# Performance work log

Hardware: AMD Instinct MI355X
Metric: run time of the kernel (lower is better)

Reference implementation:

```python
import jax, jax.numpy as jnp
import numpy as np

# GDN (gated delta-rule) linear attention, prefill path, single packed sequence,
# no initial conv/ssm state.
NUM_K_HEADS = 16
NUM_V_HEADS = 32
HEAD_K_DIM = 128
HEAD_V_DIM = 128
HIDDEN = 2048
CONV_K = 4
EPS = 1e-6
K_TOTAL = NUM_K_HEADS * HEAD_K_DIM
V_TOTAL = NUM_V_HEADS * HEAD_V_DIM
QKV_TOTAL = 2 * K_TOTAL + V_TOTAL


def setup_inputs() -> dict:
    key = jax.random.key(0)
    ks = jax.random.split(key, 9)
    T = 2048
    s = 0.02
    return {
        "hidden_states": jax.random.normal(ks[0], (T, HIDDEN), jnp.float32),
        "in_proj_qkv_weight": s * jax.random.normal(ks[1], (QKV_TOTAL, HIDDEN), jnp.float32),
        "in_proj_z_weight": s * jax.random.normal(ks[2], (V_TOTAL, HIDDEN), jnp.float32),
        "in_proj_a_weight": s * jax.random.normal(ks[3], (NUM_V_HEADS, HIDDEN), jnp.float32),
        "in_proj_b_weight": s * jax.random.normal(ks[4], (NUM_V_HEADS, HIDDEN), jnp.float32),
        "conv1d_weight": 0.1 * jax.random.normal(ks[5], (QKV_TOTAL, CONV_K), jnp.float32),
        "out_proj_weight": s * jax.random.normal(ks[6], (HIDDEN, V_TOTAL), jnp.float32),
        "norm_weight": jnp.ones((HEAD_V_DIM,), jnp.float32),
        "A_log": jnp.log(jnp.linspace(1.0, 8.0, NUM_V_HEADS, dtype=jnp.float32)),
        "dt_bias": 0.5 * jax.random.normal(ks[7], (NUM_V_HEADS,), jnp.float32),
    }


def _causal_conv1d_silu(x, w):
    # x: [T, C], w: [C, K] depthwise causal conv + SiLU
    T = x.shape[0]
    K = w.shape[1]
    xp = jnp.pad(x, ((K - 1, 0), (0, 0)))
    y = xp[0:T] * w[:, 0]
    for j in range(1, K):  # small fixed K
        y = y + xp[j:j + T] * w[:, j]
    return jax.nn.silu(y)


def _l2norm(x):
    return x / jnp.sqrt(jnp.sum(x * x, axis=-1, keepdims=True) + EPS)


def _gdn_recurrence(q, k, v, g, beta, scale):
    # q,k: [T,Hv,Dk] (l2-normed, repeated over GQA groups), v: [T,Hv,Dv]
    # g,beta: [T,Hv]. State S: [Hv,Dk,Dv]. Gated delta rule:
    #   S <- exp(g)*S ; S <- S + k^T beta (v - k S) ; o = scale * q S
    Hv, Dk = q.shape[1], q.shape[2]
    Dv = v.shape[2]

    def step(S, inp):
        q_t, k_t, v_t, g_t, b_t = inp
        S = S * jnp.exp(g_t)[:, None, None]
        pred = jnp.einsum('hk,hkv->hv', k_t, S)
        delta = b_t[:, None] * (v_t - pred)
        S = S + jnp.einsum('hk,hv->hkv', k_t, delta)
        o = jnp.einsum('hk,hkv->hv', q_t * scale, S)
        return S, o

    S0 = jnp.zeros((Hv, Dk, Dv), q.dtype)
    _, o = jax.lax.scan(step, S0, (q, k, v, g, beta))
    return o  # [T,Hv,Dv]


def reference(hidden_states, in_proj_qkv_weight, in_proj_z_weight, in_proj_a_weight,
              in_proj_b_weight, conv1d_weight, out_proj_weight, norm_weight, A_log, dt_bias):
    T = hidden_states.shape[0]
    mixed = hidden_states @ in_proj_qkv_weight.T            # [T, QKV_TOTAL]
    z = hidden_states @ in_proj_z_weight.T                  # [T, V_TOTAL]
    a = hidden_states @ in_proj_a_weight.T                  # [T, Hv]
    b = hidden_states @ in_proj_b_weight.T                  # [T, Hv]

    mixed = _causal_conv1d_silu(mixed, conv1d_weight)

    q, k, v = jnp.split(mixed, [K_TOTAL, 2 * K_TOTAL], axis=-1)
    q = q.reshape(T, NUM_K_HEADS, HEAD_K_DIM)
    k = k.reshape(T, NUM_K_HEADS, HEAD_K_DIM)
    v = v.reshape(T, NUM_V_HEADS, HEAD_V_DIM)

    # qk l2-norm in kernel, GQA repeat to v heads
    q = _l2norm(q)
    k = _l2norm(k)
    ratio = NUM_V_HEADS // NUM_K_HEADS
    q = jnp.repeat(q, ratio, axis=1)
    k = jnp.repeat(k, ratio, axis=1)

    # fused_gdn_gating: g = -exp(A_log) * softplus(a + dt_bias); beta = sigmoid(b)
    g = -jnp.exp(A_log) * jax.nn.softplus(a + dt_bias)      # [T,Hv]
    beta = jax.nn.sigmoid(b)                                # [T,Hv]

    o = _gdn_recurrence(q, k, v, g, beta, HEAD_K_DIM ** -0.5)  # [T,Hv,Dv]

    # gated RMSNorm: rmsnorm(o) * norm_weight * silu(z)
    o = o * jax.lax.rsqrt(jnp.mean(o * o, axis=-1, keepdims=True) + EPS) * norm_weight
    o = o * jax.nn.silu(z.reshape(T, NUM_V_HEADS, HEAD_V_DIM))

    return o.reshape(T, -1) @ out_proj_weight.T             # [T, HIDDEN]
```

## Files before the change

### kernel.cpp

```cpp
#include <hip/hip_runtime.h>
#include <math.h>

#define T_SEQ     2048
#define HIDDEN_D  2048
#define NUM_KH    16
#define NUM_VH    32
#define HEAD_DIM  128
#define K_TOTAL   2048
#define V_TOTAL   4096
#define QKV_TOTAL 8192
#define EPS_F     1e-6f
#define CC        32
#define NCHUNK    (T_SEQ / CC)
#define NV        8

typedef __attribute__((ext_vector_type(4))) float f32x4;
typedef __attribute__((ext_vector_type(8))) short s16x8;
typedef __attribute__((ext_vector_type(8))) unsigned short u16x8;

__device__ __forceinline__ unsigned short f2bf(float f) {
    unsigned int u = __float_as_uint(f);
    u += 0x7FFFu + ((u >> 16) & 1u);
    return (unsigned short)(u >> 16);
}

__device__ __forceinline__ float bf2f(unsigned short h) {
    return __uint_as_float((unsigned int)h << 16);
}

__global__ __launch_bounds__(256) void cast_bf16_kernel(
    const float* __restrict__ src, unsigned short* __restrict__ dst, int n4)
{
    int idx = blockIdx.x * 256 + threadIdx.x;
    if (idx >= n4) return;
    float4 v = ((const float4*)src)[idx];
    ushort4 o;
    o.x = f2bf(v.x); o.y = f2bf(v.y); o.z = f2bf(v.z); o.w = f2bf(v.w);
    ((ushort4*)dst)[idx] = o;
}

__global__ __launch_bounds__(256) void gemm_bt_bf16(
    const unsigned short* __restrict__ A, const unsigned short* __restrict__ B,
    float* __restrict__ C, int M, int N, int K)
{
    __shared__ unsigned short As[128 * 64];
    __shared__ unsigned short Bs[128 * 64];
    const int tid  = threadIdx.x;
    const int wave = tid >> 6;
    const int lane = tid & 63;
    const int m0 = blockIdx.y * 128;
    const int n0 = blockIdx.x * 128;
    const int wm = (wave >> 1) * 64;
    const int wn = (wave & 1) * 64;

    f32x4 acc[4][4];
    f32x4 zero = {0.f, 0.f, 0.f, 0.f};
#pragma unroll
    for (int i = 0; i < 4; ++i)
#pragma unroll
        for (int j = 0; j < 4; ++j) acc[i][j] = zero;

    const int srow = lane >> 3;
    const int scol = (lane & 7) * 8;
    const int rm = lane & 15;
    const int koq = (lane >> 4) * 8;

    for (int kt = 0; kt < K; kt += 64) {
#pragma unroll
        for (int l = 0; l < 4; ++l) {
            const int r0 = wave * 32 + l * 8;
            const unsigned short* ga =
                A + (size_t)(m0 + r0 + srow) * K + kt + scol;
            const unsigned short* gb =
                B + (size_t)(n0 + r0 + srow) * K + kt + scol;
            __builtin_amdgcn_global_load_lds(
                (const __attribute__((address_space(1))) void*)ga,
                (__attribute__((address_space(3))) void*)&As[r0 * 64], 16, 0, 0);
            __builtin_amdgcn_global_load_lds(
                (const __attribute__((address_space(1))) void*)gb,
                (__attribute__((address_space(3))) void*)&Bs[r0 * 64], 16, 0, 0);
        }
        __syncthreads();

#pragma unroll
        for (int ks = 0; ks < 2; ++ks) {
            const int ko = ks * 32 + koq;
            s16x8 af[4], bfr[4];
#pragma unroll
            for (int i = 0; i < 4; ++i) {
                af[i]  = *(const s16x8*)&As[(wm + i * 16 + rm) * 64 + ko];
                bfr[i] = *(const s16x8*)&Bs[(wn + i * 16 + rm) * 64 + ko];
            }
#pragma unroll
            for (int i = 0; i < 4; ++i)
#pragma unroll
                for (int j = 0; j < 4; ++j)
                    acc[i][j] = __builtin_amdgcn_mfma_f32_16x16x32_bf16(
                        af[i], bfr[j], acc[i][j], 0, 0, 0);
        }
        __syncthreads();
    }

    const int cr = (lane >> 4) * 4;
    const int ccol = lane & 15;
#pragma unroll
    for (int i = 0; i < 4; ++i)
#pragma unroll
        for (int j = 0; j < 4; ++j) {
#pragma unroll
            for (int r = 0; r < 4; ++r)
                C[(size_t)(m0 + wm + i * 16 + cr + r) * N
                  + n0 + wn + j * 16 + ccol] = acc[i][j][r];
        }
}

__global__ __launch_bounds__(256) void gemm_nt_64(
    const float* __restrict__ A, const float* __restrict__ B,
    float* __restrict__ C, int M, int N, int K)
{
    __shared__ float As[16][68];
    __shared__ float Bs[16][68];
    const int tid = threadIdx.x;
    const int m0 = blockIdx.y * 64;
    const int n0 = blockIdx.x * 64;
    const int tm = tid >> 4;
    const int tn = tid & 15;
    const int lr = tid >> 2;
    const int lc = (tid & 3) * 4;

    float acc[4][4];
#pragma unroll
    for (int i = 0; i < 4; ++i)
#pragma unroll
        for (int j = 0; j < 4; ++j) acc[i][j] = 0.f;

    for (int kt = 0; kt < K; kt += 16) {
        float4 av = *(const float4*)(A + (size_t)(m0 + lr) * K + kt + lc);
        float4 bv = *(const float4*)(B + (size_t)(n0 + lr) * K + kt + lc);
        As[lc + 0][lr] = av.x; As[lc + 1][lr] = av.y;
        As[lc + 2][lr] = av.z; As[lc + 3][lr] = av.w;
        Bs[lc + 0][lr] = bv.x; Bs[lc + 1][lr] = bv.y;
        Bs[lc + 2][lr] = bv.z; Bs[lc + 3][lr] = bv.w;
        __syncthreads();
#pragma unroll
        for (int kk = 0; kk < 16; ++kk) {
            float4 a4 = *(const float4*)&As[kk][tm * 4];
            float4 b4 = *(const float4*)&Bs[kk][tn * 4];
            float a[4] = {a4.x, a4.y, a4.z, a4.w};
            float b[4] = {b4.x, b4.y, b4.z, b4.w};
#pragma unroll
            for (int i = 0; i < 4; ++i)
#pragma unroll
                for (int j = 0; j < 4; ++j)
                    acc[i][j] = fmaf(a[i], b[j], acc[i][j]);
        }
        __syncthreads();
    }
#pragma unroll
    for (int i = 0; i < 4; ++i) {
        float4 o = make_float4(acc[i][0], acc[i][1], acc[i][2], acc[i][3]);
        *(float4*)(C + (size_t)(m0 + tm * 4 + i) * N + n0 + tn * 4) = o;
    }
}

__global__ __launch_bounds__(256) void concat_ab_kernel(
    const float* __restrict__ Wa, const float* __restrict__ Wb,
    float* __restrict__ Wab)
{
    int idx = blockIdx.x * 256 + threadIdx.x;
    int half = 16384;
    const float* src = (idx < half) ? Wa : Wb;
    int off = (idx < half) ? idx : idx - half;
    ((float4*)Wab)[idx] = ((const float4*)src)[off];
}

__global__ __launch_bounds__(256) void gating_finalize_kernel(
    const float* __restrict__ ab, const float* __restrict__ A_log,
    const float* __restrict__ dt_bias, float* __restrict__ g,
    float* __restrict__ beta)
{
    int idx = blockIdx.x * 256 + threadIdx.x;
    int t = idx >> 5, h = idx & 31;
    float a = ab[t * 64 + h] + dt_bias[h];
    float b = ab[t * 64 + 32 + h];
    float sp = (a > 20.f) ? a : log1pf(expf(a));
    g[idx] = -expf(A_log[h]) * sp;
    beta[idx] = 1.f / (1.f + expf(-b));
}

__global__ __launch_bounds__(256) void conv_v_kernel(
    const float* __restrict__ mixed, const float* __restrict__ cw,
    float* __restrict__ vb)
{
    int idx = blockIdx.x * 256 + threadIdx.x;
    int c = idx & (V_TOTAL - 1);
    int t = idx >> 12;
    int ch = 2 * K_TOTAL + c;
    const float4 w = *(const float4*)(cw + (size_t)ch * 4);
    const float* base = mixed + (size_t)t * QKV_TOTAL + ch;
    float y = w.w * base[0];
    if (t >= 1) y = fmaf(w.z, base[-QKV_TOTAL], y);
    if (t >= 2) y = fmaf(w.y, base[-2 * QKV_TOTAL], y);
    if (t >= 3) y = fmaf(w.x, base[-3 * QKV_TOTAL], y);
    vb[idx] = y / (1.f + expf(-y));
}

__global__ __launch_bounds__(64) void convqk_l2_kernel(
    const float* __restrict__ mixed, const float* __restrict__ cw,
    unsigned short* __restrict__ qk_bf)
{
    const int row = blockIdx.x;
    const int t = row >> 5;
    const int r = row & 31;
    const int lane = threadIdx.x;
    const int c = r * HEAD_DIM + lane * 2;
    const float4 w0 = *(const float4*)(cw + (size_t)c * 4);
    const float4 w1 = *(const float4*)(cw + (size_t)(c + 1) * 4);
    const float* base = mixed + (size_t)t * QKV_TOTAL + c;
    float2 x0 = *(const float2*)base;
    float y0 = w0.w * x0.x, y1 = w1.w * x0.y;
    if (t >= 1) {
        float2 x = *(const float2*)(base - QKV_TOTAL);
        y0 = fmaf(w0.z, x.x, y0); y1 = fmaf(w1.z, x.y, y1);
    }
    if (t >= 2) {
        float2 x = *(const float2*)(base - 2 * QKV_TOTAL);
        y0 = fmaf(w0.y, x.x, y0); y1 = fmaf(w1.y, x.y, y1);
    }
    if (t >= 3) {
        float2 x = *(const float2*)(base - 3 * QKV_TOTAL);
        y0 = fmaf(w0.x, x.x, y0); y1 = fmaf(w1.x, x.y, y1);
    }
    y0 = y0 / (1.f + expf(-y0));
    y1 = y1 / (1.f + expf(-y1));
    float s = y0 * y0 + y1 * y1;
    for (int off = 32; off > 0; off >>= 1) s += __shfl_down(s, off);
    s = __shfl(s, 0);
    float inv = rsqrtf(s + EPS_F);
    unsigned short* qb = qk_bf + (size_t)t * 4096 + c;
    qb[0] = f2bf(y0 * inv);
    qb[1] = f2bf(y1 * inv);
}

__global__ __launch_bounds__(256) void gdn_p1(
    const unsigned short* __restrict__ qk_bf, const float* __restrict__ g,
    const float* __restrict__ beta, unsigned short* __restrict__ PTbuf,
    unsigned short* __restrict__ K2buf, float* __restrict__ lam_g,
    float* __restrict__ bet_g)
{
    __shared__ float Kn[CC][132];
    __shared__ float Qn[CC][132];
    __shared__ float Wm[CC][33];
    __shared__ float Tld[CC][36];
    __shared__ float Pm[CC][33];
    __shared__ float Trl[CC][33];
    __shared__ float cums[CC];
    __shared__ float betas[CC];
    __shared__ float rlS[CC];

    const int tid = threadIdx.x;
    const int h   = blockIdx.x;
    const int cix = blockIdx.y;
    const int t0  = cix * CC;
    const int kh  = h >> 1;
    const float scale = 0.08838834764831845f;
    const size_t mb = ((size_t)cix * NUM_VH + h);
    const size_t sb = mb * CC;

    if (tid < CC) {
        float x = g[(size_t)(t0 + tid) * NUM_VH + h];
        float bv = beta[(size_t)(t0 + tid) * NUM_VH + h];
#pragma unroll
        for (int off = 1; off < 32; off <<= 1) {
            float n = __shfl_up(x, off);
            if (tid >= off) x += n;
        }
        cums[tid] = x;
        betas[tid] = bv;
        float c31 = __shfl(x, 31);
        lam_g[sb + tid] = expf(x);
        bet_g[sb + tid] = bv;
        rlS[tid] = expf(c31 - x);
    }
#pragma unroll
    for (int p = 0; p < 2; ++p) {
        int idx = p * 256 + tid;
        int i = idx >> 4, ch = (idx & 15) * 8;
        const unsigned short* qr =
            qk_bf + (size_t)(t0 + i) * 4096 + kh * HEAD_DIM + ch;
        u16x8 q8 = *(const u16x8*)qr;
        u16x8 k8 = *(const u16x8*)(qr + K_TOTAL);
        float4 kf0, kf1, qf0, qf1;
        kf0.x = bf2f(k8[0]); kf0.y = bf2f(k8[1]);
        kf0.z = bf2f(k8[2]); kf0.w = bf2f(k8[3]);
        kf1.x = bf2f(k8[4]); kf1.y = bf2f(k8[5]);
        kf1.z = bf2f(k8[6]); kf1.w = bf2f(k8[7]);
        qf0.x = bf2f(q8[0]) * scale; qf0.y = bf2f(q8[1]) * scale;
        qf0.z = bf2f(q8[2]) * scale; qf0.w = bf2f(q8[3]) * scale;
        qf1.x = bf2f(q8[4]) * scale; qf1.y = bf2f(q8[5]) * scale;
        qf1.z = bf2f(q8[6]) * scale; qf1.w = bf2f(q8[7]) * scale;
        *(float4*)&Kn[i][ch]     = kf0;
        *(float4*)&Kn[i][ch + 4] = kf1;
        *(float4*)&Qn[i][ch]     = qf0;
        *(float4*)&Qn[i][ch + 4] = qf1;
    }
    __syncthreads();

    {
        const int i0 = (tid >> 4) * 2, j0 = (tid & 15) * 2;
        float wa[2][2] = {{0.f, 0.f}, {0.f, 0.f}};
        float pa[2][2] = {{0.f, 0.f}, {0.f, 0.f}};
        for (int k = 0; k < HEAD_DIM; k += 4) {
            float4 a0 = *(const float4*)&Kn[i0][k];
            float4 a1 = *(const float4*)&Kn[i0 + 1][k];
            float4 b0 = *(const float4*)&Kn[j0][k];
            float4 b1 = *(const float4*)&Kn[j0 + 1][k];
            float4 c0 = *(const float4*)&Qn[i0][k];
            float4 c1 = *(const float4*)&Qn[i0 + 1][k];
            const float* ap0 = (const float*)&a0;
            const float* ap1 = (const float*)&a1;
            const float* bp0 = (const float*)&b0;
            const float* bp1 = (const float*)&b1;
            const float* cp0 = (const float*)&c0;
            const float* cp1 = (const float*)&c1;
#pragma unroll
            for (int cc = 0; cc < 4; ++cc) {
                wa[0][0] = fmaf(ap0[cc], bp0[cc], wa[0][0]);
                wa[0][1] = fmaf(ap0[cc], bp1[cc], wa[0][1]);
                wa[1][0] = fmaf(ap1[cc], bp0[cc], wa[1][0]);
                wa[1][1] = fmaf(ap1[cc], bp1[cc], wa[1][1]);
                pa[0][0] = fmaf(cp0[cc], bp0[cc], pa[0][0]);
                pa[0][1] = fmaf(cp0[cc], bp1[cc], pa[0][1]);
                pa[1][0] = fmaf(cp1[cc], bp0[cc], pa[1][0]);
                pa[1][1] = fmaf(cp1[cc], bp1[cc], pa[1][1]);
            }
        }
#pragma unroll
        for (int di = 0; di < 2; ++di)
#pragma unroll
            for (int dj = 0; dj < 2; ++dj) {
                int i = i0 + di, j = j0 + dj;
                float rr = expf(fminf(cums[i] - cums[j], 0.f));
                Wm[i][j] = (j < i) ? betas[i] * rr * wa[di][dj] : 0.f;
                Pm[i][j] = (j <= i) ? rr * pa[di][dj] : 0.f;
            }
    }
    __syncthreads();

    {
        const int col = tid >> 3, tk = tid & 7;
        if (tk == 0) Tld[0][col] = (col == 0) ? 1.f : 0.f;
        for (int i = 1; i < CC; ++i) {
            float part = 0.f;
            for (int j = tk; j < i; j += 8)
                part = fmaf(Wm[i][j], Tld[j][col], part);
            part += __shfl_xor(part, 4);
            part += __shfl_xor(part, 2);
            part += __shfl_xor(part, 1);
            if (tk == 0) Tld[i][col] = ((i == col) ? 1.f : 0.f) - part;
        }
    }
    __syncthreads();

    {
        const int i = tid >> 3, j0 = (tid & 7) * 4;
        const float r = rlS[i];
#pragma unroll
        for (int e = 0; e < 4; ++e)
            Trl[i][j0 + e] = Tld[i][j0 + e] * r;
        float4 accp = {0.f, 0.f, 0.f, 0.f};
        for (int m = 0; m < CC; ++m) {
            float pv = Pm[i][m];
            float4 tv = *(const float4*)&Tld[m][j0];
            accp.x = fmaf(pv, tv.x, accp.x);
            accp.y = fmaf(pv, tv.y, accp.y);
            accp.z = fmaf(pv, tv.z, accp.z);
            accp.w = fmaf(pv, tv.w, accp.w);
        }
        ushort4 pt4;
        pt4.x = f2bf(accp.x); pt4.y = f2bf(accp.y);
        pt4.z = f2bf(accp.z); pt4.w = f2bf(accp.w);
        *(ushort4*)(PTbuf + mb * (CC * CC) + tid * 4) = pt4;
    }
    __syncthreads();

    {
        const int m0 = tid >> 3;
        const int q  = (tid & 7) * 4;
        float acc[4][4];
#pragma unroll
        for (int c = 0; c < 4; ++c)
#pragma unroll
            for (int e = 0; e < 4; ++e) acc[c][e] = 0.f;
        for (int j = 0; j < CC; ++j) {
            float t = Trl[j][m0];
#pragma unroll
            for (int c = 0; c < 4; ++c) {
                float4 a = *(const float4*)&Kn[j][q + 32 * c];
                acc[c][0] = fmaf(t, a.x, acc[c][0]);
                acc[c][1] = fmaf(t, a.y, acc[c][1]);
                acc[c][2] = fmaf(t, a.z, acc[c][2]);
                acc[c][3] = fmaf(t, a.w, acc[c][3]);
            }
        }
        unsigned short* kout =
            K2buf + mb * (CC * HEAD_DIM) + m0 * HEAD_DIM + q;
#pragma unroll
        for (int c = 0; c < 4; ++c) {
            ushort4 o4;
            o4.x = f2bf(acc[c][0]); o4.y = f2bf(acc[c][1]);
            o4.z = f2bf(acc[c][2]); o4.w = f2bf(acc[c][3]);
            *(ushort4*)(kout + 32 * c) = o4;
        }
    }
}

__global__ __launch_bounds__(256, 2) void gdn_p2(
    const float* __restrict__ vb, const unsigned short* __restrict__ qk_bf,
    const unsigned short* __restrict__ PTbuf,
    const unsigned short* __restrict__ K2buf, const float* __restrict__ lam_g,
    const float* __restrict__ bet_g, float* __restrict__ o)
{
    __shared__ unsigned short Kn[CC][128];
    __shared__ unsigned short Qn[CC][128];
    __shared__ unsigned short K2l[2][CC][128];
    __shared__ float PTl[2][CC][36];
    __shared__ float Sm[HEAD_DIM][NV + 2];
    __shared__ float Dl[CC][NV + 2];
    __shared__ float lamS[2][CC], betS[2][CC];

    const int tid = threadIdx.x;
    const int wv  = tid >> 6;
    const int ln  = tid & 63;
    const int h   = blockIdx.x >> 4;
    const int V0  = (blockIdx.x & 15) * NV;
    const int kh  = h >> 1;
    const float scale = 0.08838834764831845f;

    const int ri = tid >> 3;
    const int rn = (tid & 3) * 2;
    const int hh = (tid >> 2) & 1;
    const int rx2 = ri & 3;

    const int fk = (tid >> 3) * 4;
    const int sn = tid & 7;

    const int drow = ln >> 4;
    const int dc   = ln & 15;

#define DMA_KQ(T0)                                                            \
    {                                                                         \
        _Pragma("unroll")                                                     \
        for (int p = 0; p < 2; ++p) {                                         \
            const int i = p * 16 + wv * 4 + drow;                             \
            const int sc = 2 * ((dc >> 1) ^ (i & 3)) + (dc & 1);              \
            const unsigned short* sq = qk_bf + (size_t)((T0) + i) * 4096      \
                                       + kh * HEAD_DIM + sc * 8;              \
            __builtin_amdgcn_global_load_lds(                                 \
                (const __attribute__((address_space(1))) void*)(sq + K_TOTAL),\
                (__attribute__((address_space(3))) void*)                     \
                    &Kn[p * 16 + wv * 4][0], 16, 0, 0);                       \
            __builtin_amdgcn_global_load_lds(                                 \
                (const __attribute__((address_space(1))) void*)sq,            \
                (__attribute__((address_space(3))) void*)                     \
                    &Qn[p * 16 + wv * 4][0], 16, 0, 0);                       \
        }                                                                     \
    }

#define DMA_K2(MB, BUF)                                                       \
    {                                                                         \
        _Pragma("unroll")                                                     \
        for (int p = 0; p < 2; ++p) {                                         \
            const unsigned short* sk = K2buf + (MB) * (CC * HEAD_DIM)         \
                                       + p * 2048 + wv * 512 + ln * 8;        \
            __builtin_amdgcn_global_load_lds(                                 \
                (const __attribute__((address_space(1))) void*)sk,            \
                (__attribute__((address_space(3))) void*)                     \
                    &K2l[BUF][p * 16 + wv * 4][0], 16, 0, 0);                 \
        }                                                                     \
    }

#pragma unroll
    for (int c = 0; c < 4; ++c) Sm[fk + c][sn] = 0.f;

    DMA_KQ(0);
    DMA_K2((size_t)h, 0);
    {
        ushort4 pt0 = *(const ushort4*)(PTbuf + (size_t)h * (CC * CC) + tid * 4);
        float4 pf;
        pf.x = bf2f(pt0.x); pf.y = bf2f(pt0.y);
        pf.z = bf2f(pt0.z); pf.w = bf2f(pt0.w);
        *(float4*)&PTl[0][tid >> 3][(tid & 7) * 4] = pf;
        if (tid < CC) {
            lamS[0][tid] = lam_g[(size_t)h * CC + tid];
            betS[0][tid] = bet_g[(size_t)h * CC + tid];
        }
    }
    float2 vR = *(const float2*)(vb + (size_t)ri * V_TOTAL
                                 + h * HEAD_DIM + V0 + rn);

    int cur = 0;
    for (int cix = 0; cix < NCHUNK; ++cix) {
        const int t0 = cix * CC;
        __syncthreads();

        const float lam = lamS[cur][ri];
        const float bet = betS[cur][ri];
        float r1x = 0.f, r1y = 0.f, r2x = 0.f, r2y = 0.f;
#pragma unroll
        for (int kk = 0; kk < 8; ++kk) {
            const int pc = (2 * (kk ^ rx2) + hh) * 8;
            const int cl = kk * 16 + hh * 8;
            u16x8 kv = *(const u16x8*)&Kn[ri][pc];
            u16x8 qv = *(const u16x8*)&Qn[ri][pc];
#pragma unroll
            for (int c8 = 0; c8 < 8; ++c8) {
                float kf = bf2f(kv[c8]);
                float qf = bf2f(qv[c8]);
                float2 s = *(const float2*)&Sm[cl + c8][rn];
                r1x = fmaf(kf, s.x, r1x);
                r1y = fmaf(kf, s.y, r1y);
                r2x = fmaf(qf, s.x, r2x);
                r2y = fmaf(qf, s.y, r2y);
            }
        }
        r1x += __shfl_xor(r1x, 4);
        r1y += __shfl_xor(r1y, 4);
        r2x += __shfl_xor(r2x, 4);
        r2y += __shfl_xor(r2y, 4);
        {
            float dlx = bet * (vR.x - lam * r1x);
            float dly = bet * (vR.y - lam * r1y);
            if (hh == 0) { Dl[ri][rn] = dlx; Dl[ri][rn + 1] = dly; }
        }
        const float lsc = lam * scale;
        float ox = r2x * lsc, oy = r2y * lsc;
        __syncthreads();

        const int nxt = cur ^ 1;
        ushort4 ptN; float lamN = 0.f, betN = 0.f; float2 vN;
        const int more = (cix + 1 < NCHUNK);
        if (more) {
            const int t0n = t0 + CC;
            const size_t mbn = (size_t)(cix + 1) * NUM_VH + h;
            DMA_KQ(t0n);
            DMA_K2(mbn, nxt);
            ptN = *(const ushort4*)(PTbuf + mbn * (CC * CC) + tid * 4);
            if (tid < CC) {
                lamN = lam_g[mbn * CC + tid];
                betN = bet_g[mbn * CC + tid];
            }
            vN = *(const float2*)(vb + (size_t)(t0n + ri) * V_TOTAL
                                  + h * HEAD_DIM + V0 + rn);
        }

        {
            for (int j = 0; j < CC; ++j) {
                float p = PTl[cur][ri][j];
                float2 d = *(const float2*)&Dl[j][rn];
                ox = fmaf(p, d.x, ox);
                oy = fmaf(p, d.y, oy);
            }
            if (hh == 0)
                *(float2*)(o + (size_t)(t0 + ri) * V_TOTAL + h * HEAD_DIM + V0 + rn)
                    = make_float2(ox, oy);
        }

        {
            const float lamL = lamS[cur][CC - 1];
            float s0 = lamL * Sm[fk + 0][sn];
            float s1 = lamL * Sm[fk + 1][sn];
            float s2 = lamL * Sm[fk + 2][sn];
            float s3 = lamL * Sm[fk + 3][sn];
            for (int j = 0; j < CC; ++j) {
                ushort4 kk = *(const ushort4*)&K2l[cur][j][fk];
                float d = Dl[j][sn];
                s0 = fmaf(bf2f(kk.x), d, s0);
                s1 = fmaf(bf2f(kk.y), d, s1);
                s2 = fmaf(bf2f(kk.z), d, s2);
                s3 = fmaf(bf2f(kk.w), d, s3);
            }
            Sm[fk + 0][sn] = s0;
            Sm[fk + 1][sn] = s1;
            Sm[fk + 2][sn] = s2;
            Sm[fk + 3][sn] = s3;
        }

        if (more) {
            float4 pf;
            pf.x = bf2f(ptN.x); pf.y = bf2f(ptN.y);
            pf.z = bf2f(ptN.z); pf.w = bf2f(ptN.w);
            *(float4*)&PTl[nxt][tid >> 3][(tid & 7) * 4] = pf;
            if (tid < CC) { lamS[nxt][tid] = lamN; betS[nxt][tid] = betN; }
            vR = vN;
        }
        cur = nxt;
    }
#undef DMA_KQ
#undef DMA_K2
}

__global__ __launch_bounds__(64) void rmsnorm_gate_kernel(
    float* __restrict__ o, const float* __restrict__ z,
    const float* __restrict__ nw)
{
    const int row = blockIdx.x;
    float* p = o + (size_t)row * HEAD_DIM;
    const float* zp = z + (size_t)row * HEAD_DIM;
    const int lane = threadIdx.x;
    float2 v = *(float2*)(p + lane * 2);
    float s = v.x * v.x + v.y * v.y;
    for (int off = 32; off > 0; off >>= 1) s += __shfl_down(s, off);
    s = __shfl(s, 0);
    float inv = rsqrtf(s * (1.f / HEAD_DIM) + EPS_F);
    float2 zv = *(float2*)(zp + lane * 2);
    float2 wv = *(const float2*)(nw + lane * 2);
    v.x = v.x * inv * wv.x * (zv.x / (1.f + expf(-zv.x)));
    v.y = v.y * inv * wv.y * (zv.y / (1.f + expf(-zv.y)));
    *(float2*)(p + lane * 2) = v;
}

extern "C" void kernel_launch(void* const* d_in, const int* in_sizes, int n_in,
                              void* d_out, int out_size, void* d_ws,
                              size_t ws_size, hipStream_t stream)
{
    const float* hs    = (const float*)d_in[0];
    const float* Wqkv  = (const float*)d_in[1];
    const float* Wz    = (const float*)d_in[2];
    const float* Wa    = (const float*)d_in[3];
    const float* Wb    = (const float*)d_in[4];
    const float* cw    = (const float*)d_in[5];
    const float* Wout  = (const float*)d_in[6];
    const float* nw    = (const float*)d_in[7];
    const float* A_log = (const float*)d_in[8];
    const float* dtb   = (const float*)d_in[9];
    float* out = (float*)d_out;

    float* F     = (float*)d_ws;
    float* mixed = F;
    float* ob    = F;
    unsigned short* PTbuf = (unsigned short*)(F + (size_t)8388608);
    unsigned short* K2buf = (unsigned short*)(F + (size_t)9437184);
    float* lam_b = F + (size_t)13631488;
    float* bet_b = F + (size_t)13697024;
    unsigned short* hs_bf   = (unsigned short*)(F + (size_t)16777216);
    unsigned short* Wqkv_bf = (unsigned short*)(F + (size_t)18874368);
    float* vb = F + (size_t)16777216;
    unsigned short* qk_bf = (unsigned short*)(F + (size_t)25165824);
    unsigned short* Wz_bf   = (unsigned short*)(F + (size_t)27262976);
    float* Wab = F + (size_t)27262976;
    float* ab  = F + (size_t)27394048;
    float* zb  = F + (size_t)33554432;
    unsigned short* ob_bf   = (unsigned short*)(F + (size_t)33554432);
    unsigned short* Wout_bf = (unsigned short*)(F + (size_t)37748736);
    float* gb = F + (size_t)41943040;
    float* bb = F + (size_t)42008576;

    cast_bf16_kernel<<<1048576 / 256, 256, 0, stream>>>(hs, hs_bf, 1048576);
    cast_bf16_kernel<<<4194304 / 256, 256, 0, stream>>>(Wqkv, Wqkv_bf, 4194304);
    cast_bf16_kernel<<<2097152 / 256, 256, 0, stream>>>(Wz, Wz_bf, 2097152);
    gemm_bt_bf16<<<dim3(QKV_TOTAL / 128, T_SEQ / 128), 256, 0, stream>>>(
        hs_bf, Wqkv_bf, mixed, T_SEQ, QKV_TOTAL, HIDDEN_D);
    gemm_bt_bf16<<<dim3(V_TOTAL / 128, T_SEQ / 128), 256, 0, stream>>>(
        hs_bf, Wz_bf, zb, T_SEQ, V_TOTAL, HIDDEN_D);
    concat_ab_kernel<<<32768 / 256, 256, 0, stream>>>(Wa, Wb, Wab);
    gemm_nt_64<<<dim3(1, T_SEQ / 64), 256, 0, stream>>>(
        hs, Wab, ab, T_SEQ, 64, HIDDEN_D);
    gating_finalize_kernel<<<(T_SEQ * NUM_VH) / 256, 256, 0, stream>>>(
        ab, A_log, dtb, gb, bb);
    conv_v_kernel<<<(T_SEQ * V_TOTAL) / 256, 256, 0, stream>>>(
        mixed, cw, vb);
    convqk_l2_kernel<<<T_SEQ * 32, 64, 0, stream>>>(mixed, cw, qk_bf);
    gdn_p1<<<dim3(NUM_VH, NCHUNK), 256, 0, stream>>>(
        qk_bf, gb, bb, PTbuf, K2buf, lam_b, bet_b);
    gdn_p2<<<NUM_VH * (HEAD_DIM / NV), 256, 0, stream>>>(
        vb, qk_bf, PTbuf, K2buf, lam_b, bet_b, ob);
    rmsnorm_gate_kernel<<<T_SEQ * NUM_VH, 64, 0, stream>>>(ob, zb, nw);
    cast_bf16_kernel<<<2097152 / 256, 256, 0, stream>>>(ob, ob_bf, 2097152);
    cast_bf16_kernel<<<2097152 / 256, 256, 0, stream>>>(Wout, Wout_bf, 2097152);
    gemm_bt_bf16<<<dim3(HIDDEN_D / 128, T_SEQ / 128), 256, 0, stream>>>(
        ob_bf, Wout_bf, out, T_SEQ, HIDDEN_D, V_TOTAL);
}
```

Baseline: 929.4 us.

## Fuse input casts, fold bf16 cast into rmsnorm, remap gdn_p2 threads

Merges the three fp32-to-bf16 input casts into a single launch and has the gated RMSNorm kernel write bf16 directly, which removes a separate cast kernel and one fp32 round trip of the output buffer. In the recurrence kernel, each thread now handles two rows and a quarter of the K dimension, so each Sm load is reused across two rows, at the cost of a two-step shuffle reduction and more registers. The ob_bf buffer moves to the PTbuf region, which is free once gdn_p2 has finished.

```diff
diff --git a/kernel.cpp b/kernel.cpp
--- a/kernel.cpp
+++ b/kernel.cpp
@@ -37,6 +37,22 @@
     ushort4 o;
     o.x = f2bf(v.x); o.y = f2bf(v.y); o.z = f2bf(v.z); o.w = f2bf(v.w);
     ((ushort4*)dst)[idx] = o;
+}
+
+__global__ __launch_bounds__(256) void cast3_kernel(
+    const float* __restrict__ hs, const float* __restrict__ Wqkv,
+    const float* __restrict__ Wz, unsigned short* __restrict__ hs_bf,
+    unsigned short* __restrict__ Wqkv_bf, unsigned short* __restrict__ Wz_bf)
+{
+    int idx = blockIdx.x * 256 + threadIdx.x;
+    const float* src; unsigned short* dst; int off;
+    if (idx < 1048576)      { src = hs;   dst = hs_bf;   off = idx; }
+    else if (idx < 5242880) { src = Wqkv; dst = Wqkv_bf; off = idx - 1048576; }
+    else                    { src = Wz;   dst = Wz_bf;   off = idx - 5242880; }
+    float4 v = ((const float4*)src)[off];
+    ushort4 o;
+    o.x = f2bf(v.x); o.y = f2bf(v.y); o.z = f2bf(v.z); o.w = f2bf(v.w);
+    ((ushort4*)dst)[off] = o;
 }
 
 __global__ __launch_bounds__(256) void gemm_bt_bf16(
@@ -437,10 +453,10 @@
     const int kh  = h >> 1;
     const float scale = 0.08838834764831845f;
 
-    const int ri = tid >> 3;
-    const int rn = (tid & 3) * 2;
-    const int hh = (tid >> 2) & 1;
-    const int rx2 = ri & 3;
+    const int hh  = tid & 3;
+    const int rn2 = ((tid >> 2) & 3) * 2;
+    const int rp  = tid >> 4;
+    const int rx  = rp & 3;
 
     const int fk = (tid >> 3) * 4;
     const int sn = tid & 7;
@@ -496,49 +512,66 @@
             betS[0][tid] = bet_g[(size_t)h * CC + tid];
         }
     }
-    float2 vR = *(const float2*)(vb + (size_t)ri * V_TOTAL
-                                 + h * HEAD_DIM + V0 + rn);
+    float2 vR0 = *(const float2*)(vb + (size_t)rp * V_TOTAL
+                                  + h * HEAD_DIM + V0 + rn2);
+    float2 vR1 = *(const float2*)(vb + (size_t)(rp + 16) * V_TOTAL
+                                  + h * HEAD_DIM + V0 + rn2);
 
     int cur = 0;
     for (int cix = 0; cix < NCHUNK; ++cix) {
         const int t0 = cix * CC;
         __syncthreads();
 
-        const float lam = lamS[cur][ri];
-        const float bet = betS[cur][ri];
-        float r1x = 0.f, r1y = 0.f, r2x = 0.f, r2y = 0.f;
-#pragma unroll
-        for (int kk = 0; kk < 8; ++kk) {
-            const int pc = (2 * (kk ^ rx2) + hh) * 8;
-            const int cl = kk * 16 + hh * 8;
-            u16x8 kv = *(const u16x8*)&Kn[ri][pc];
-            u16x8 qv = *(const u16x8*)&Qn[ri][pc];
+        const float lam0 = lamS[cur][rp];
+        const float lam1 = lamS[cur][rp + 16];
+        const float bet0 = betS[cur][rp];
+        const float bet1 = betS[cur][rp + 16];
+        float r1x0 = 0.f, r1y0 = 0.f, r2x0 = 0.f, r2y0 = 0.f;
+        float r1x1 = 0.f, r1y1 = 0.f, r2x1 = 0.f, r2y1 = 0.f;
+#pragma unroll
+        for (int j = 0; j < 4; ++j) {
+            const int c  = 4 * j + hh;
+            const int pc = (2 * ((c >> 1) ^ rx) + (c & 1)) * 8;
+            u16x8 kv0 = *(const u16x8*)&Kn[rp][pc];
+            u16x8 qv0 = *(const u16x8*)&Qn[rp][pc];
+            u16x8 kv1 = *(const u16x8*)&Kn[rp + 16][pc];
+            u16x8 qv1 = *(const u16x8*)&Qn[rp + 16][pc];
+            const int kb = c * 8;
 #pragma unroll
             for (int c8 = 0; c8 < 8; ++c8) {
-                float kf = bf2f(kv[c8]);
-                float qf = bf2f(qv[c8]);
-                float2 s = *(const float2*)&Sm[cl + c8][rn];
-                r1x = fmaf(kf, s.x, r1x);
-                r1y = fmaf(kf, s.y, r1y);
-                r2x = fmaf(qf, s.x, r2x);
-                r2y = fmaf(qf, s.y, r2y);
-            }
-        }
-        r1x += __shfl_xor(r1x, 4);
-        r1y += __shfl_xor(r1y, 4);
-        r2x += __shfl_xor(r2x, 4);
-        r2y += __shfl_xor(r2y, 4);
+                float2 s = *(const float2*)&Sm[kb + c8][rn2];
+                float k0 = bf2f(kv0[c8]), q0 = bf2f(qv0[c8]);
+                float k1 = bf2f(kv1[c8]), q1 = bf2f(qv1[c8]);
+                r1x0 = fmaf(k0, s.x, r1x0); r1y0 = fmaf(k0, s.y, r1y0);
+                r2x0 = fmaf(q0, s.x, r2x0); r2y0 = fmaf(q0, s.y, r2y0);
+                r1x1 = fmaf(k1, s.x, r1x1); r1y1 = fmaf(k1, s.y, r1y1);
+                r2x1 = fmaf(q1, s.x, r2x1); r2y1 = fmaf(q1, s.y, r2y1);
+            }
+        }
+        r1x0 += __shfl_xor(r1x0, 1); r1x0 += __shfl_xor(r1x0, 2);
+        r1y0 += __shfl_xor(r1y0, 1); r1y0 += __shfl_xor(r1y0, 2);
+        r2x0 += __shfl_xor(r2x0, 1); r2x0 += __shfl_xor(r2x0, 2);
+        r2y0 += __shfl_xor(r2y0, 1); r2y0 += __shfl_xor(r2y0, 2);
+        r1x1 += __shfl_xor(r1x1, 1); r1x1 += __shfl_xor(r1x1, 2);
+        r1y1 += __shfl_xor(r1y1, 1); r1y1 += __shfl_xor(r1y1, 2);
+        r2x1 += __shfl_xor(r2x1, 1); r2x1 += __shfl_xor(r2x1, 2);
+        r2y1 += __shfl_xor(r2y1, 1); r2y1 += __shfl_xor(r2y1, 2);
         {
-            float dlx = bet * (vR.x - lam * r1x);
-            float dly = bet * (vR.y - lam * r1y);
-            if (hh == 0) { Dl[ri][rn] = dlx; Dl[ri][rn + 1] = dly; }
-        }
-        const float lsc = lam * scale;
-        float ox = r2x * lsc, oy = r2y * lsc;
+            float dlx0 = bet0 * (vR0.x - lam0 * r1x0);
+            float dly0 = bet0 * (vR0.y - lam0 * r1y0);
+            float dlx1 = bet1 * (vR1.x - lam1 * r1x1);
+            float dly1 = bet1 * (vR1.y - lam1 * r1y1);
+            if (hh == 0) {
+                Dl[rp][rn2] = dlx0; Dl[rp][rn2 + 1] = dly0;
+                Dl[rp + 16][rn2] = dlx1; Dl[rp + 16][rn2 + 1] = dly1;
+            }
+        }
+        float ox0 = r2x0 * lam0 * scale, oy0 = r2y0 * lam0 * scale;
+        float ox1 = r2x1 * lam1 * scale, oy1 = r2y1 * lam1 * scale;
         __syncthreads();
 
         const int nxt = cur ^ 1;
-        ushort4 ptN; float lamN = 0.f, betN = 0.f; float2 vN;
+        ushort4 ptN; float lamN = 0.f, betN = 0.f; float2 vN0, vN1;
         const int more = (cix + 1 < NCHUNK);
         if (more) {
             const int t0n = t0 + CC;
@@ -550,20 +583,26 @@
                 lamN = lam_g[mbn * CC + tid];
                 betN = bet_g[mbn * CC + tid];
             }
-            vN = *(const float2*)(vb + (size_t)(t0n + ri) * V_TOTAL
-                                  + h * HEAD_DIM + V0 + rn);
+            vN0 = *(const float2*)(vb + (size_t)(t0n + rp) * V_TOTAL
+                                   + h * HEAD_DIM + V0 + rn2);
+            vN1 = *(const float2*)(vb + (size_t)(t0n + rp + 16) * V_TOTAL
+                                   + h * HEAD_DIM + V0 + rn2);
         }
 
         {
             for (int j = 0; j < CC; ++j) {
-                float p = PTl[cur][ri][j];
-                float2 d = *(const float2*)&Dl[j][rn];
-                ox = fmaf(p, d.x, ox);
-                oy = fmaf(p, d.y, oy);
-            }
-            if (hh == 0)
-                *(float2*)(o + (size_t)(t0 + ri) * V_TOTAL + h * HEAD_DIM + V0 + rn)
-                    = make_float2(ox, oy);
+                float2 d = *(const float2*)&Dl[j][rn2];
+                float p0 = PTl[cur][rp][j];
+                float p1 = PTl[cur][rp + 16][j];
+                ox0 = fmaf(p0, d.x, ox0); oy0 = fmaf(p0, d.y, oy0);
+                ox1 = fmaf(p1, d.x, ox1); oy1 = fmaf(p1, d.y, oy1);
+            }
+            if (hh == 0) {
+                *(float2*)(o + (size_t)(t0 + rp) * V_TOTAL
+                           + h * HEAD_DIM + V0 + rn2) = make_float2(ox0, oy0);
+                *(float2*)(o + (size_t)(t0 + rp + 16) * V_TOTAL
+                           + h * HEAD_DIM + V0 + rn2) = make_float2(ox1, oy1);
+            }
         }
 
         {
@@ -592,7 +631,7 @@
             pf.z = bf2f(ptN.z); pf.w = bf2f(ptN.w);
             *(float4*)&PTl[nxt][tid >> 3][(tid & 7) * 4] = pf;
             if (tid < CC) { lamS[nxt][tid] = lamN; betS[nxt][tid] = betN; }
-            vR = vN;
+            vR0 = vN0; vR1 = vN1;
         }
         cur = nxt;
     }
@@ -601,23 +640,25 @@
 }
 
 __global__ __launch_bounds__(64) void rmsnorm_gate_kernel(
-    float* __restrict__ o, const float* __restrict__ z,
-    const float* __restrict__ nw)
+    const float* __restrict__ o, const float* __restrict__ z,
+    const float* __restrict__ nw, unsigned short* __restrict__ ob_bf)
 {
     const int row = blockIdx.x;
-    float* p = o + (size_t)row * HEAD_DIM;
+    const float* p = o + (size_t)row * HEAD_DIM;
     const float* zp = z + (size_t)row * HEAD_DIM;
     const int lane = threadIdx.x;
-    float2 v = *(float2*)(p + lane * 2);
+    float2 v = *(const float2*)(p + lane * 2);
     float s = v.x * v.x + v.y * v.y;
     for (int off = 32; off > 0; off >>= 1) s += __shfl_down(s, off);
     s = __shfl(s, 0);
     float inv = rsqrtf(s * (1.f / HEAD_DIM) + EPS_F);
-    float2 zv = *(float2*)(zp + lane * 2);
+    float2 zv = *(const float2*)(zp + lane * 2);
     float2 wv = *(const float2*)(nw + lane * 2);
     v.x = v.x * inv * wv.x * (zv.x / (1.f + expf(-zv.x)));
     v.y = v.y * inv * wv.y * (zv.y / (1.f + expf(-zv.y)));
-    *(float2*)(p + lane * 2) = v;
+    unsigned short* q = ob_bf + (size_t)row * HEAD_DIM + lane * 2;
+    q[0] = f2bf(v.x);
+    q[1] = f2bf(v.y);
 }
 
 extern "C" void kernel_launch(void* const* d_in, const int* in_sizes, int n_in,
@@ -640,6 +681,7 @@
     float* mixed = F;
     float* ob    = F;
     unsigned short* PTbuf = (unsigned short*)(F + (size_t)8388608);
+    unsigned short* ob_bf = (unsigned short*)(F + (size_t)8388608);
     unsigned short* K2buf = (unsigned short*)(F + (size_t)9437184);
     float* lam_b = F + (size_t)13631488;
     float* bet_b = F + (size_t)13697024;
@@ -651,14 +693,12 @@
     float* Wab = F + (size_t)27262976;
     float* ab  = F + (size_t)27394048;
     float* zb  = F + (size_t)33554432;
-    unsigned short* ob_bf   = (unsigned short*)(F + (size_t)33554432);
     unsigned short* Wout_bf = (unsigned short*)(F + (size_t)37748736);
     float* gb = F + (size_t)41943040;
     float* bb = F + (size_t)42008576;
 
-    cast_bf16_kernel<<<1048576 / 256, 256, 0, stream>>>(hs, hs_bf, 1048576);
-    cast_bf16_kernel<<<4194304 / 256, 256, 0, stream>>>(Wqkv, Wqkv_bf, 4194304);
-    cast_bf16_kernel<<<2097152 / 256, 256, 0, stream>>>(Wz, Wz_bf, 2097152);
+    cast3_kernel<<<7340032 / 256, 256, 0, stream>>>(
+        hs, Wqkv, Wz, hs_bf, Wqkv_bf, Wz_bf);
     gemm_bt_bf16<<<dim3(QKV_TOTAL / 128, T_SEQ / 128), 256, 0, stream>>>(
         hs_bf, Wqkv_bf, mixed, T_SEQ, QKV_TOTAL, HIDDEN_D);
     gemm_bt_bf16<<<dim3(V_TOTAL / 128, T_SEQ / 128), 256, 0, stream>>>(
@@ -675,8 +715,7 @@
         qk_bf, gb, bb, PTbuf, K2buf, lam_b, bet_b);
     gdn_p2<<<NUM_VH * (HEAD_DIM / NV), 256, 0, stream>>>(
         vb, qk_bf, PTbuf, K2buf, lam_b, bet_b, ob);
-    rmsnorm_gate_kernel<<<T_SEQ * NUM_VH, 64, 0, stream>>>(ob, zb, nw);
-    cast_bf16_kernel<<<2097152 / 256, 256, 0, stream>>>(ob, ob_bf, 2097152);
+    rmsnorm_gate_kernel<<<T_SEQ * NUM_VH, 64, 0, stream>>>(ob, zb, nw, ob_bf);
     cast_bf16_kernel<<<2097152 / 256, 256, 0, stream>>>(Wout, Wout_bf, 2097152);
     gemm_bt_bf16<<<dim3(HIDDEN_D / 128, T_SEQ / 128), 256, 0, stream>>>(
         ob_bf, Wout_bf, out, T_SEQ, HIDDEN_D, V_TOTAL);
```

New measurement: 941.1 us. About the same (+1.3%).
